# Performance work log

Measured on AMD Instinct MI355X. Metric: run time of the kernel, lower is better.

The kernel has to match this reference:

```python
import jax, jax.numpy as jnp
import numpy as np

B, T, E, D = 64, 512, 1024, 1024  # batch, enc timesteps, enc hidden, dec hidden


def setup_inputs() -> dict:
    key = jax.random.key(0)
    ks = jax.random.split(key, 9)
    s = lambda fan_in: 1.0 / np.sqrt(fan_in)
    return {
        "hidden": jax.random.normal(ks[0], (B, D), jnp.float32),
        "decoder_out": jax.random.normal(ks[1], (B, D), jnp.float32),
        "encoder_states": jax.random.normal(ks[2], (T, B, E), jnp.float32),
        # attn: Linear(D+E -> 2E)
        "Wa": jax.random.uniform(ks[3], (2 * E, D + E), jnp.float32, -s(D + E), s(D + E)),
        "ba": jax.random.uniform(ks[4], (2 * E,), jnp.float32, -s(D + E), s(D + E)),
        # attn2: Linear(2E -> 1)
        "w2": jax.random.uniform(ks[5], (1, 2 * E), jnp.float32, -s(2 * E), s(2 * E)),
        "b2": jax.random.uniform(ks[6], (1,), jnp.float32, -s(2 * E), s(2 * E)),
        # attn_combine: Linear(D+E -> D)
        "Wc": jax.random.uniform(ks[7], (D, D + E), jnp.float32, -s(D + E), s(D + E)),
        "bc": jax.random.uniform(ks[8], (D,), jnp.float32, -s(D + E), s(D + E)),
    }


def reference(hidden, decoder_out, encoder_states, Wa, ba, w2, b2, Wc, bc):
    d = hidden.shape[1]
    # attn(cat(hidden, enc_t)) = hidden @ Wa[:, :D].T + enc_t @ Wa[:, D:].T + ba
    h_proj = hidden @ Wa[:, :d].T + ba                      # [B, 2E]
    e_proj = jnp.einsum('tbe,fe->tbf', encoder_states, Wa[:, d:])  # [T, B, 2E]
    act = jnp.tanh(h_proj[None, :, :] + e_proj)             # [T, B, 2E]
    scores = jnp.einsum('tbf,f->bt', act, w2[0]) + b2[0]    # [B, T]
    weights = jax.nn.softmax(scores, axis=-1)               # softmax over timesteps
    # weighted sum of encoder states: [B, E]
    applied = jnp.einsum('bt,tbe->be', weights, encoder_states)
    combined = jnp.concatenate([decoder_out, applied], axis=1)  # [B, D+E]
    out = jnp.tanh(combined @ Wc.T + bc)                    # [B, D]
    return out, applied
```

## Files before the change

kernel.cpp:

```cpp
#include <hip/hip_runtime.h>
#include <hip/hip_bf16.h>

#define BB 64
#define TT 512
#define EE 1024
#define DD 1024

typedef __attribute__((ext_vector_type(8))) short s16x8;
typedef __attribute__((ext_vector_type(4))) float f32x4;

__device__ __forceinline__ float bf2f(unsigned short u) {
    unsigned int x = ((unsigned int)u) << 16;
    return __builtin_bit_cast(float, x);
}
__device__ __forceinline__ unsigned short f2bf(float f) {
    unsigned int u = __builtin_bit_cast(unsigned int, f);
    u += 0x7FFF + ((u >> 16) & 1);
    return (unsigned short)(u >> 16);
}
__device__ __forceinline__ float tanh_fast(float x) {
    x = fminf(fmaxf(x, -15.f), 15.f);
    float e = __expf(2.f * x);
    return (e - 1.f) / (e + 1.f);
}

__device__ __forceinline__ int tile_slot(int row, int g) {
    return (row >> 4) * 128 + (g >> 2) * 64 + (g & 3) * 16 + (row & 15);
}

__global__ __launch_bounds__(256) void conv_encS_kernel(
    const float* __restrict__ enc, unsigned short* __restrict__ encS)
{
    const int tm  = blockIdx.x;
    const int tk  = blockIdx.y;
    const int tid = threadIdx.x;
    unsigned short* dst = encS + ((size_t)tm * 16 + tk) * 8192;

#pragma unroll
    for (int it = 0; it < 4; ++it) {
        int cidx = it * 256 + tid;
        int row  = cidx >> 3;
        int g    = cidx & 7;
        const float* src = enc + (size_t)(tm * 128 + row) * 1024 + tk * 64 + g * 8;
        float4 v0 = ((const float4*)src)[0];
        float4 v1 = ((const float4*)src)[1];
        short c[8];
        c[0] = (short)f2bf(v0.x); c[1] = (short)f2bf(v0.y);
        c[2] = (short)f2bf(v0.z); c[3] = (short)f2bf(v0.w);
        c[4] = (short)f2bf(v1.x); c[5] = (short)f2bf(v1.y);
        c[6] = (short)f2bf(v1.z); c[7] = (short)f2bf(v1.w);
        *(s16x8*)&dst[tile_slot(row, g) * 8] = *(s16x8*)c;
    }
}

__global__ __launch_bounds__(256) void conv_waS_kernel(
    const float* __restrict__ Wa, unsigned short* __restrict__ WaS)
{
    const int tn  = blockIdx.x;
    const int tk  = blockIdx.y;
    const int tid = threadIdx.x;
    unsigned short* dst = WaS + ((size_t)tn * 16 + tk) * 8192;

#pragma unroll
    for (int it = 0; it < 4; ++it) {
        int cidx = it * 256 + tid;
        int row  = cidx >> 3;
        int g    = cidx & 7;
        const float* src = Wa + (size_t)(tn * 128 + row) * 2048 + 1024 + tk * 64 + g * 8;
        float4 v0 = ((const float4*)src)[0];
        float4 v1 = ((const float4*)src)[1];
        short c[8];
        c[0] = (short)f2bf(v0.x); c[1] = (short)f2bf(v0.y);
        c[2] = (short)f2bf(v0.z); c[3] = (short)f2bf(v0.w);
        c[4] = (short)f2bf(v1.x); c[5] = (short)f2bf(v1.y);
        c[6] = (short)f2bf(v1.z); c[7] = (short)f2bf(v1.w);
        *(s16x8*)&dst[tile_slot(row, g) * 8] = *(s16x8*)c;
    }
}

__global__ __launch_bounds__(256) void hproj_kernel(
    const float* __restrict__ hidden,
    const float* __restrict__ Wa,
    const float* __restrict__ ba,
    float* __restrict__ hp)
{
    __shared__ float sW[8 * 1024];
    const int tid  = threadIdx.x;
    const int lane = tid & 63;
    const int wave = tid >> 6;
    const int f0   = blockIdx.x * 8;

#pragma unroll
    for (int i = 0; i < 8; ++i) {
        int idx = i * 256 + tid;
        int fi  = idx >> 8;
        int c4  = idx & 255;
        ((float4*)sW)[idx] = *(const float4*)(Wa + (size_t)(f0 + fi) * 2048 + c4 * 4);
    }
    __syncthreads();

    for (int bi = 0; bi < 16; ++bi) {
        int b = wave * 16 + bi;
        float h[16];
#pragma unroll
        for (int j = 0; j < 16; ++j) h[j] = hidden[b * 1024 + lane + 64 * j];
#pragma unroll
        for (int fi = 0; fi < 8; ++fi) {
            float s = 0.f;
#pragma unroll
            for (int j = 0; j < 16; ++j) s += h[j] * sW[fi * 1024 + lane + 64 * j];
#pragma unroll
            for (int m = 32; m; m >>= 1) s += __shfl_xor(s, m);
            if (lane == 0) hp[(f0 + fi) * 64 + b] = s + ba[f0 + fi];
        }
    }
}

__global__ __launch_bounds__(256, 2) void gemm_scores(
    const unsigned short* __restrict__ encS,
    const unsigned short* __restrict__ WaS,
    const float* __restrict__ hp,
    const float* __restrict__ w2,
    float* __restrict__ scoresP)
{
    __shared__ float rowAcc[128];

    const int tid  = threadIdx.x;
    const int bm   = blockIdx.x;
    const int bn   = blockIdx.y;
    const int lane = tid & 63;
    const int wave = tid >> 6;
    const int wm   = wave >> 1;
    const int wn   = wave & 1;
    const int c    = lane & 15;
    const int quad = lane >> 4;

    if (tid < 128) rowAcc[tid] = 0.f;

    f32x4 acc[4][8];
#pragma unroll
    for (int mi = 0; mi < 4; ++mi)
#pragma unroll
        for (int ni = 0; ni < 8; ++ni)
#pragma unroll
            for (int r = 0; r < 4; ++r) acc[mi][ni][r] = 0.f;

    const unsigned short* aBase = encS + (size_t)bm * 16 * 8192 + wm * 4096 + lane * 8;
    const unsigned short* bBase = WaS + ((size_t)(bn * 2 + wn) * 16) * 8192 + lane * 8;

    s16x8 aF[2][4], bF[2][8];

#pragma unroll
    for (int mi = 0; mi < 4; ++mi)
        aF[0][mi] = *(const s16x8*)(aBase + mi * 1024);
#pragma unroll
    for (int ni = 0; ni < 8; ++ni)
        bF[0][ni] = *(const s16x8*)(bBase + ni * 1024);

#pragma unroll
    for (int h = 0; h < 32; ++h) {
        const int cur = h & 1;
        const int nxt = cur ^ 1;
        if (h < 31) {
            const int h1 = h + 1;
            const unsigned short* pa = aBase + (h1 >> 1) * 8192 + (h1 & 1) * 512;
            const unsigned short* pb = bBase + (h1 >> 1) * 8192 + (h1 & 1) * 512;
#pragma unroll
            for (int mi = 0; mi < 4; ++mi)
                aF[nxt][mi] = *(const s16x8*)(pa + mi * 1024);
#pragma unroll
            for (int ni = 0; ni < 8; ++ni)
                bF[nxt][ni] = *(const s16x8*)(pb + ni * 1024);
        }
#pragma unroll
        for (int mi = 0; mi < 4; ++mi)
#pragma unroll
            for (int ni = 0; ni < 8; ++ni)
                acc[mi][ni] = __builtin_amdgcn_mfma_f32_16x16x32_bf16(
                    aF[cur][mi], bF[cur][ni], acc[mi][ni], 0, 0, 0);
    }

    __syncthreads();

    float w2v[8];
#pragma unroll
    for (int ni = 0; ni < 8; ++ni)
        w2v[ni] = w2[bn * 256 + wn * 128 + ni * 16 + c];

#pragma unroll
    for (int mi = 0; mi < 4; ++mi) {
        int lrow0 = wm * 64 + mi * 16 + quad * 4;
        int b0    = (bm * 128 + lrow0) & 63;
        f32x4 hp4[8];
#pragma unroll
        for (int ni = 0; ni < 8; ++ni)
            hp4[ni] = *(const f32x4*)&hp[(bn * 256 + wn * 128 + ni * 16 + c) * 64 + b0];
#pragma unroll
        for (int r = 0; r < 4; ++r) {
            float s = 0.f;
#pragma unroll
            for (int ni = 0; ni < 8; ++ni)
                s += tanh_fast(acc[mi][ni][r] + hp4[ni][r]) * w2v[ni];
            s += __shfl_xor(s, 1);
            s += __shfl_xor(s, 2);
            s += __shfl_xor(s, 4);
            s += __shfl_xor(s, 8);
            if (c == 0) atomicAdd(&rowAcc[lrow0 + r], s);
        }
    }
    __syncthreads();
    if (tid < 128) {
        int grow = bm * 128 + tid;
        int b = grow & 63;
        int t = grow >> 6;
        scoresP[((size_t)bn * 64 + b) * 512 + t] = rowAcc[tid];
    }
}

__global__ __launch_bounds__(256) void softmax_kernel(
    const float* __restrict__ scoresP, float* __restrict__ weights)
{
    __shared__ float wmax[4];
    __shared__ float wsum[4];
    const int b   = blockIdx.x;
    const int tid = threadIdx.x;

    float v0 = 0.f, v1 = 0.f;
#pragma unroll
    for (int p = 0; p < 8; ++p) {
        const float* row = scoresP + ((size_t)p * 64 + b) * 512;
        v0 += row[tid];
        v1 += row[tid + 256];
    }
    float m = fmaxf(v0, v1);
#pragma unroll
    for (int s = 32; s; s >>= 1) m = fmaxf(m, __shfl_xor(m, s));
    if ((tid & 63) == 0) wmax[tid >> 6] = m;
    __syncthreads();
    m = fmaxf(fmaxf(wmax[0], wmax[1]), fmaxf(wmax[2], wmax[3]));

    float e0 = __expf(v0 - m), e1 = __expf(v1 - m);
    float s = e0 + e1;
#pragma unroll
    for (int t = 32; t; t >>= 1) s += __shfl_xor(s, t);
    if ((tid & 63) == 0) wsum[tid >> 6] = s;
    __syncthreads();
    float inv = 1.f / (wsum[0] + wsum[1] + wsum[2] + wsum[3]);
    float* row = weights + (size_t)b * 512;
    row[tid]       = e0 * inv;
    row[tid + 256] = e1 * inv;
}

__global__ __launch_bounds__(256) void applied_part_kernel(
    const float* __restrict__ enc,
    const float* __restrict__ w,
    float* __restrict__ part)
{
    __shared__ float red[128 * 8];
    const int tc  = blockIdx.x;
    const int b   = blockIdx.y;
    const int tid = threadIdx.x;
    const int eo  = tid & 127;
    const int th  = tid >> 7;
    const int e0  = eo * 8;

    float a[8];
#pragma unroll
    for (int j = 0; j < 8; ++j) a[j] = 0.f;

    for (int it = 0; it < 16; ++it) {
        int t = tc * 32 + th * 16 + it;
        float wt = w[b * TT + t];
        const float* src = enc + ((size_t)(t * BB + b)) * EE + e0;
        float4 v0 = ((const float4*)src)[0];
        float4 v1 = ((const float4*)src)[1];
        a[0] += wt * v0.x; a[1] += wt * v0.y; a[2] += wt * v0.z; a[3] += wt * v0.w;
        a[4] += wt * v1.x; a[5] += wt * v1.y; a[6] += wt * v1.z; a[7] += wt * v1.w;
    }
    if (th == 1) {
#pragma unroll
        for (int j = 0; j < 8; ++j) red[eo * 8 + j] = a[j];
    }
    __syncthreads();
    if (th == 0) {
        float* dst = part + ((size_t)tc * 64 + b) * 1024 + e0;
#pragma unroll
        for (int j = 0; j < 8; ++j) dst[j] = a[j] + red[eo * 8 + j];
    }
}

__global__ __launch_bounds__(256) void applied_reduce_kernel(
    const float* __restrict__ part, float* __restrict__ out_applied)
{
    int idx = blockIdx.x * 256 + threadIdx.x;
    float s = 0.f;
#pragma unroll
    for (int tc = 0; tc < 16; ++tc) s += part[tc * 65536 + idx];
    out_applied[idx] = s;
}

__global__ __launch_bounds__(256) void combine_kernel(
    const float* __restrict__ dec,
    const float* applied,
    const float* __restrict__ Wc,
    const float* __restrict__ bc,
    float* out0)
{
    const int g    = blockIdx.x * 4 + (threadIdx.x >> 6);
    const int lane = threadIdx.x & 63;
    const int d    = g >> 6;
    const int b    = g & 63;

    const float4* wc4 = (const float4*)Wc + (size_t)d * 512;
    const float4* de4 = (const float4*)dec + (size_t)b * 256;
    const float4* ap4 = (const float4*)applied + (size_t)b * 256;

    float s = 0.f;
#pragma unroll
    for (int j = 0; j < 4; ++j) {
        float4 a = de4[j * 64 + lane];
        float4 wv = wc4[j * 64 + lane];
        s += a.x * wv.x + a.y * wv.y + a.z * wv.z + a.w * wv.w;
    }
#pragma unroll
    for (int j = 0; j < 4; ++j) {
        float4 a = ap4[j * 64 + lane];
        float4 wv = wc4[256 + j * 64 + lane];
        s += a.x * wv.x + a.y * wv.y + a.z * wv.z + a.w * wv.w;
    }
#pragma unroll
    for (int m = 32; m; m >>= 1) s += __shfl_xor(s, m);
    if (lane == 0) out0[b * DD + d] = tanh_fast(s + bc[d]);
}

extern "C" void kernel_launch(void* const* d_in, const int* in_sizes, int n_in,
                              void* d_out, int out_size, void* d_ws, size_t ws_size,
                              hipStream_t stream) {
    const float* hidden = (const float*)d_in[0];
    const float* dec    = (const float*)d_in[1];
    const float* enc    = (const float*)d_in[2];
    const float* Wa     = (const float*)d_in[3];
    const float* ba     = (const float*)d_in[4];
    const float* w2     = (const float*)d_in[5];
    const float* Wc     = (const float*)d_in[7];
    const float* bc     = (const float*)d_in[8];
    float* out = (float*)d_out;

    unsigned short* encS = (unsigned short*)d_ws;
    unsigned short* WaS  = encS + (size_t)33554432;
    float* hp      = (float*)(WaS + (size_t)2097152);
    float* scoresP = hp + 131072;
    float* weights = scoresP + 262144;
    float* part    = weights + 32768;

    dim3 gc(256, 16);
    conv_encS_kernel<<<gc, 256, 0, stream>>>(enc, encS);
    dim3 gw(16, 16);
    conv_waS_kernel<<<gw, 256, 0, stream>>>(Wa, WaS);
    hproj_kernel<<<256, 256, 0, stream>>>(hidden, Wa, ba, hp);
    dim3 g2(256, 8);
    gemm_scores<<<g2, 256, 0, stream>>>(encS, WaS, hp, w2, scoresP);
    softmax_kernel<<<BB, 256, 0, stream>>>(scoresP, weights);
    dim3 g3(16, 64);
    applied_part_kernel<<<g3, 256, 0, stream>>>(enc, weights, part);
    applied_reduce_kernel<<<256, 256, 0, stream>>>(part, out + BB * DD);
    combine_kernel<<<16384, 256, 0, stream>>>(dec, out + BB * DD, Wc, bc, out);
}
```

Before: 571.1 us.

## Fuse prep kernels and merge softmax into atomic applied reduction

Merges the encoder/Wa bf16 conversion, h-projection and zeroing of the applied output into one launch. Each block of the applied kernel now recomputes the softmax for its batch row and keeps its 64-timestep slice of weights in shared memory. It then accumulates the weighted encoder sum straight into the output with atomics, dropping the separate softmax, partial-sum buffer and reduce kernel. This removes launch overhead and intermediate traffic, at the cost of recomputing the softmax 8 times per row and issuing float atomics.

New measurement: 570.1 us. No clear change (-0.2%).

```diff
diff --git a/kernel.cpp b/kernel.cpp
--- a/kernel.cpp
+++ b/kernel.cpp
@@ -28,91 +28,92 @@
     return (row >> 4) * 128 + (g >> 2) * 64 + (g & 3) * 16 + (row & 15);
 }
 
-__global__ __launch_bounds__(256) void conv_encS_kernel(
-    const float* __restrict__ enc, unsigned short* __restrict__ encS)
+__global__ __launch_bounds__(256) void prep_kernel(
+    const float* __restrict__ enc,
+    const float* __restrict__ Wa,
+    const float* __restrict__ hidden,
+    const float* __restrict__ ba,
+    unsigned short* __restrict__ encS,
+    unsigned short* __restrict__ WaS,
+    float* __restrict__ hp,
+    float* __restrict__ out_applied)
 {
-    const int tm  = blockIdx.x;
-    const int tk  = blockIdx.y;
+    const int blk = blockIdx.x;
     const int tid = threadIdx.x;
-    unsigned short* dst = encS + ((size_t)tm * 16 + tk) * 8192;
-
-#pragma unroll
-    for (int it = 0; it < 4; ++it) {
-        int cidx = it * 256 + tid;
-        int row  = cidx >> 3;
-        int g    = cidx & 7;
-        const float* src = enc + (size_t)(tm * 128 + row) * 1024 + tk * 64 + g * 8;
-        float4 v0 = ((const float4*)src)[0];
-        float4 v1 = ((const float4*)src)[1];
-        short c[8];
-        c[0] = (short)f2bf(v0.x); c[1] = (short)f2bf(v0.y);
-        c[2] = (short)f2bf(v0.z); c[3] = (short)f2bf(v0.w);
-        c[4] = (short)f2bf(v1.x); c[5] = (short)f2bf(v1.y);
-        c[6] = (short)f2bf(v1.z); c[7] = (short)f2bf(v1.w);
-        *(s16x8*)&dst[tile_slot(row, g) * 8] = *(s16x8*)c;
-    }
-}
-
-__global__ __launch_bounds__(256) void conv_waS_kernel(
-    const float* __restrict__ Wa, unsigned short* __restrict__ WaS)
-{
-    const int tn  = blockIdx.x;
-    const int tk  = blockIdx.y;
-    const int tid = threadIdx.x;
-    unsigned short* dst = WaS + ((size_t)tn * 16 + tk) * 8192;
-
-#pragma unroll
-    for (int it = 0; it < 4; ++it) {
-        int cidx = it * 256 + tid;
-        int row  = cidx >> 3;
-        int g    = cidx & 7;
-        const float* src = Wa + (size_t)(tn * 128 + row) * 2048 + 1024 + tk * 64 + g * 8;
-        float4 v0 = ((const float4*)src)[0];
-        float4 v1 = ((const float4*)src)[1];
-        short c[8];
-        c[0] = (short)f2bf(v0.x); c[1] = (short)f2bf(v0.y);
-        c[2] = (short)f2bf(v0.z); c[3] = (short)f2bf(v0.w);
-        c[4] = (short)f2bf(v1.x); c[5] = (short)f2bf(v1.y);
-        c[6] = (short)f2bf(v1.z); c[7] = (short)f2bf(v1.w);
-        *(s16x8*)&dst[tile_slot(row, g) * 8] = *(s16x8*)c;
-    }
-}
-
-__global__ __launch_bounds__(256) void hproj_kernel(
-    const float* __restrict__ hidden,
-    const float* __restrict__ Wa,
-    const float* __restrict__ ba,
-    float* __restrict__ hp)
-{
-    __shared__ float sW[8 * 1024];
-    const int tid  = threadIdx.x;
-    const int lane = tid & 63;
-    const int wave = tid >> 6;
-    const int f0   = blockIdx.x * 8;
-
-#pragma unroll
-    for (int i = 0; i < 8; ++i) {
-        int idx = i * 256 + tid;
-        int fi  = idx >> 8;
-        int c4  = idx & 255;
-        ((float4*)sW)[idx] = *(const float4*)(Wa + (size_t)(f0 + fi) * 2048 + c4 * 4);
-    }
-    __syncthreads();
-
-    for (int bi = 0; bi < 16; ++bi) {
-        int b = wave * 16 + bi;
-        float h[16];
-#pragma unroll
-        for (int j = 0; j < 16; ++j) h[j] = hidden[b * 1024 + lane + 64 * j];
-#pragma unroll
-        for (int fi = 0; fi < 8; ++fi) {
-            float s = 0.f;
-#pragma unroll
-            for (int j = 0; j < 16; ++j) s += h[j] * sW[fi * 1024 + lane + 64 * j];
-#pragma unroll
-            for (int m = 32; m; m >>= 1) s += __shfl_xor(s, m);
-            if (lane == 0) hp[(f0 + fi) * 64 + b] = s + ba[f0 + fi];
-        }
+
+    if (blk < 4096) {
+        const int tm = blk >> 4;
+        const int tk = blk & 15;
+        unsigned short* dst = encS + ((size_t)tm * 16 + tk) * 8192;
+#pragma unroll
+        for (int it = 0; it < 4; ++it) {
+            int cidx = it * 256 + tid;
+            int row  = cidx >> 3;
+            int g    = cidx & 7;
+            const float* src = enc + (size_t)(tm * 128 + row) * 1024 + tk * 64 + g * 8;
+            float4 v0 = ((const float4*)src)[0];
+            float4 v1 = ((const float4*)src)[1];
+            short c[8];
+            c[0] = (short)f2bf(v0.x); c[1] = (short)f2bf(v0.y);
+            c[2] = (short)f2bf(v0.z); c[3] = (short)f2bf(v0.w);
+            c[4] = (short)f2bf(v1.x); c[5] = (short)f2bf(v1.y);
+            c[6] = (short)f2bf(v1.z); c[7] = (short)f2bf(v1.w);
+            *(s16x8*)&dst[tile_slot(row, g) * 8] = *(s16x8*)c;
+        }
+    } else if (blk < 4352) {
+        const int t  = blk - 4096;
+        const int tn = t >> 4;
+        const int tk = t & 15;
+        unsigned short* dst = WaS + ((size_t)tn * 16 + tk) * 8192;
+#pragma unroll
+        for (int it = 0; it < 4; ++it) {
+            int cidx = it * 256 + tid;
+            int row  = cidx >> 3;
+            int g    = cidx & 7;
+            const float* src = Wa + (size_t)(tn * 128 + row) * 2048 + 1024 + tk * 64 + g * 8;
+            float4 v0 = ((const float4*)src)[0];
+            float4 v1 = ((const float4*)src)[1];
+            short c[8];
+            c[0] = (short)f2bf(v0.x); c[1] = (short)f2bf(v0.y);
+            c[2] = (short)f2bf(v0.z); c[3] = (short)f2bf(v0.w);
+            c[4] = (short)f2bf(v1.x); c[5] = (short)f2bf(v1.y);
+            c[6] = (short)f2bf(v1.z); c[7] = (short)f2bf(v1.w);
+            *(s16x8*)&dst[tile_slot(row, g) * 8] = *(s16x8*)c;
+        }
+    } else if (blk < 4608) {
+        __shared__ float sW[8 * 1024];
+        const int lane = tid & 63;
+        const int wave = tid >> 6;
+        const int f0   = (blk - 4352) * 8;
+#pragma unroll
+        for (int i = 0; i < 8; ++i) {
+            int idx = i * 256 + tid;
+            int fi  = idx >> 8;
+            int c4  = idx & 255;
+            ((float4*)sW)[idx] = *(const float4*)(Wa + (size_t)(f0 + fi) * 2048 + c4 * 4);
+        }
+        __syncthreads();
+        for (int bi = 0; bi < 16; ++bi) {
+            int b = wave * 16 + bi;
+            float h[16];
+#pragma unroll
+            for (int j = 0; j < 16; ++j) h[j] = hidden[b * 1024 + lane + 64 * j];
+#pragma unroll
+            for (int fi = 0; fi < 8; ++fi) {
+                float s = 0.f;
+#pragma unroll
+                for (int j = 0; j < 16; ++j) s += h[j] * sW[fi * 1024 + lane + 64 * j];
+#pragma unroll
+                for (int m = 32; m; m >>= 1) s += __shfl_xor(s, m);
+                if (lane == 0) hp[(f0 + fi) * 64 + b] = s + ba[f0 + fi];
+            }
+        }
+    } else {
+        int idx = (blk - 4608) * 256 + tid;
+        float4 z = {0.f, 0.f, 0.f, 0.f};
+#pragma unroll
+        for (int j = 0; j < 4; ++j)
+            ((float4*)out_applied)[idx * 4 + j] = z;
     }
 }
 
@@ -217,12 +218,15 @@
     }
 }
 
-__global__ __launch_bounds__(256) void softmax_kernel(
-    const float* __restrict__ scoresP, float* __restrict__ weights)
+__global__ __launch_bounds__(256) void applied_kernel(
+    const float* __restrict__ enc,
+    const float* __restrict__ scoresP,
+    float* __restrict__ out_applied)
 {
-    __shared__ float wmax[4];
-    __shared__ float wsum[4];
-    const int b   = blockIdx.x;
+    __shared__ float red[4];
+    __shared__ float wts[64];
+    const int tc  = blockIdx.x;
+    const int b   = blockIdx.y;
     const int tid = threadIdx.x;
 
     float v0 = 0.f, v1 = 0.f;
@@ -235,68 +239,43 @@
     float m = fmaxf(v0, v1);
 #pragma unroll
     for (int s = 32; s; s >>= 1) m = fmaxf(m, __shfl_xor(m, s));
-    if ((tid & 63) == 0) wmax[tid >> 6] = m;
-    __syncthreads();
-    m = fmaxf(fmaxf(wmax[0], wmax[1]), fmaxf(wmax[2], wmax[3]));
-
+    if ((tid & 63) == 0) red[tid >> 6] = m;
+    __syncthreads();
+    m = fmaxf(fmaxf(red[0], red[1]), fmaxf(red[2], red[3]));
+    __syncthreads();
     float e0 = __expf(v0 - m), e1 = __expf(v1 - m);
     float s = e0 + e1;
 #pragma unroll
     for (int t = 32; t; t >>= 1) s += __shfl_xor(s, t);
-    if ((tid & 63) == 0) wsum[tid >> 6] = s;
-    __syncthreads();
-    float inv = 1.f / (wsum[0] + wsum[1] + wsum[2] + wsum[3]);
-    float* row = weights + (size_t)b * 512;
-    row[tid]       = e0 * inv;
-    row[tid + 256] = e1 * inv;
-}
-
-__global__ __launch_bounds__(256) void applied_part_kernel(
-    const float* __restrict__ enc,
-    const float* __restrict__ w,
-    float* __restrict__ part)
-{
-    __shared__ float red[128 * 8];
-    const int tc  = blockIdx.x;
-    const int b   = blockIdx.y;
-    const int tid = threadIdx.x;
-    const int eo  = tid & 127;
-    const int th  = tid >> 7;
-    const int e0  = eo * 8;
-
+    if ((tid & 63) == 0) red[tid >> 6] = s;
+    __syncthreads();
+    float inv = 1.f / (red[0] + red[1] + red[2] + red[3]);
+    if ((tid & 255) >= (tc * 64 & 255)) {}
+    if (tid >= tc * 64 && tid < tc * 64 + 64 && tc < 4)
+        wts[tid - tc * 64] = e0 * inv;
+    if (tid + 256 >= tc * 64 && tid + 256 < tc * 64 + 64 && tc >= 4)
+        wts[tid + 256 - tc * 64] = e1 * inv;
+    __syncthreads();
+
+    const int eo = tid & 127;
+    const int th = tid >> 7;
+    const int e0i = eo * 8;
     float a[8];
 #pragma unroll
     for (int j = 0; j < 8; ++j) a[j] = 0.f;
-
-    for (int it = 0; it < 16; ++it) {
-        int t = tc * 32 + th * 16 + it;
-        float wt = w[b * TT + t];
-        const float* src = enc + ((size_t)(t * BB + b)) * EE + e0;
-        float4 v0 = ((const float4*)src)[0];
-        float4 v1 = ((const float4*)src)[1];
-        a[0] += wt * v0.x; a[1] += wt * v0.y; a[2] += wt * v0.z; a[3] += wt * v0.w;
-        a[4] += wt * v1.x; a[5] += wt * v1.y; a[6] += wt * v1.z; a[7] += wt * v1.w;
-    }
-    if (th == 1) {
-#pragma unroll
-        for (int j = 0; j < 8; ++j) red[eo * 8 + j] = a[j];
-    }
-    __syncthreads();
-    if (th == 0) {
-        float* dst = part + ((size_t)tc * 64 + b) * 1024 + e0;
-#pragma unroll
-        for (int j = 0; j < 8; ++j) dst[j] = a[j] + red[eo * 8 + j];
-    }
-}
-
-__global__ __launch_bounds__(256) void applied_reduce_kernel(
-    const float* __restrict__ part, float* __restrict__ out_applied)
-{
-    int idx = blockIdx.x * 256 + threadIdx.x;
-    float s = 0.f;
-#pragma unroll
-    for (int tc = 0; tc < 16; ++tc) s += part[tc * 65536 + idx];
-    out_applied[idx] = s;
+    for (int it = 0; it < 32; ++it) {
+        int tl = th * 32 + it;
+        int t  = tc * 64 + tl;
+        float wt = wts[tl];
+        const float* src = enc + ((size_t)(t * BB + b)) * EE + e0i;
+        float4 u0 = ((const float4*)src)[0];
+        float4 u1 = ((const float4*)src)[1];
+        a[0] += wt * u0.x; a[1] += wt * u0.y; a[2] += wt * u0.z; a[3] += wt * u0.w;
+        a[4] += wt * u1.x; a[5] += wt * u1.y; a[6] += wt * u1.z; a[7] += wt * u1.w;
+    }
+    float* dst = out_applied + (size_t)b * 1024 + e0i;
+#pragma unroll
+    for (int j = 0; j < 8; ++j) atomicAdd(&dst[j], a[j]);
 }
 
 __global__ __launch_bounds__(256) void combine_kernel(
@@ -350,19 +329,13 @@
     unsigned short* WaS  = encS + (size_t)33554432;
     float* hp      = (float*)(WaS + (size_t)2097152);
     float* scoresP = hp + 131072;
-    float* weights = scoresP + 262144;
-    float* part    = weights + 32768;
-
-    dim3 gc(256, 16);
-    conv_encS_kernel<<<gc, 256, 0, stream>>>(enc, encS);
-    dim3 gw(16, 16);
-    conv_waS_kernel<<<gw, 256, 0, stream>>>(Wa, WaS);
-    hproj_kernel<<<256, 256, 0, stream>>>(hidden, Wa, ba, hp);
+
+    float* out_applied = out + BB * DD;
+
+    prep_kernel<<<4624, 256, 0, stream>>>(enc, Wa, hidden, ba, encS, WaS, hp, out_applied);
     dim3 g2(256, 8);
     gemm_scores<<<g2, 256, 0, stream>>>(encS, WaS, hp, w2, scoresP);
-    softmax_kernel<<<BB, 256, 0, stream>>>(scoresP, weights);
-    dim3 g3(16, 64);
-    applied_part_kernel<<<g3, 256, 0, stream>>>(enc, weights, part);
-    applied_reduce_kernel<<<256, 256, 0, stream>>>(part, out + BB * DD);
-    combine_kernel<<<16384, 256, 0, stream>>>(dec, out + BB * DD, Wc, bc, out);
-}
+    dim3 g3(8, 64);
+    applied_kernel<<<g3, 256, 0, stream>>>(enc, scoresP, out_applied);
+    combine_kernel<<<16384, 256, 0, stream>>>(dec, out_applied, Wc, bc, out);
+}
```
